# Kernel optimization log

Measured on AMD Instinct MI355X. Metric: run time of the kernel, lower is better.

The kernel has to match this reference:

```python
import jax, jax.numpy as jnp
import numpy as np

BS, K, VOCAB = 128, 8, 50257

def setup_inputs() -> dict:
    key = jax.random.key(0)
    k1, k2, k3, k4 = jax.random.split(key, 4)
    logits = jax.random.normal(k1, (BS * K + BS, VOCAB), dtype=jnp.float32)
    temperatures = jax.random.uniform(k2, (BS,), minval=0.5, maxval=1.5, dtype=jnp.float32)
    draft_token_ids = jax.random.randint(k3, (BS, K), 0, VOCAB)
    dlogits = jax.random.normal(k4, (BS * K, VOCAB), dtype=jnp.float32)
    draft_probs = jax.nn.softmax(dlogits, axis=-1)  # valid draft distribution per row
    return {"draft_token_ids": draft_token_ids, "logits": logits,
            "temperatures": temperatures, "draft_probs": draft_probs}

def reference(draft_token_ids, logits, temperatures, draft_probs):
    bs, k = draft_token_ids.shape
    vocab = logits.shape[-1]
    n_draft = bs * k
    nkey = jax.random.key(42)
    ku, kg_rec, kg_bonus = jax.random.split(nkey, 3)

    # --- bonus token sampling (inner `sampler`): categorical over softmax(logits/temp)
    # via the Gumbel-max trick (equivalent to torch.multinomial on the softmax probs)
    bonus_logits = logits[n_draft:] / temperatures[:, None]            # [bs, vocab]
    g_bonus = jax.random.gumbel(kg_bonus, (bs, vocab), dtype=jnp.float32)
    bonus_ids = jnp.argmax(bonus_logits + g_bonus, axis=-1)           # [bs]

    # --- target probabilities for draft positions
    target_logits = logits[:n_draft].reshape(bs, k, vocab) / temperatures[:, None, None]
    target_probs = jax.nn.softmax(target_logits, axis=-1)              # [bs,k,vocab]
    dprobs = draft_probs.reshape(bs, k, vocab)

    # per-position probs of the proposed draft token
    p_t = jnp.take_along_axis(target_probs, draft_token_ids[..., None], axis=-1)[..., 0]
    p_d = jnp.take_along_axis(dprobs, draft_token_ids[..., None], axis=-1)[..., 0]
    accept_prob = jnp.where(p_d > 0.0,
                            jnp.minimum(1.0, p_t / jnp.maximum(p_d, 1e-30)),
                            0.0)                                       # [bs,k]
    u = jax.random.uniform(ku, (bs, k), dtype=jnp.float32)
    accept = u <= accept_prob                                          # [bs,k]

    # accepted prefix length: number of leading accepts
    prefix = jnp.cumprod(accept.astype(jnp.int32), axis=1)
    n_acc = prefix.sum(axis=1)                                         # [bs] in [0,k]

    # --- recovery sampling: multinomial over clamp(target - draft, 0), renormalized;
    # fall back to target_probs if residual mass is zero. Gumbel-max on log weights
    # is invariant to normalization, so no explicit division by the mass is needed.
    rec = jnp.maximum(target_probs - dprobs, 0.0)                      # [bs,k,vocab]
    mass = rec.sum(axis=-1, keepdims=True)
    rec_dist = jnp.where(mass > 0.0, rec, target_probs)
    g_rec = jax.random.gumbel(kg_rec, (bs, k, vocab), dtype=jnp.float32)
    recovered = jnp.argmax(jnp.log(jnp.maximum(rec_dist, 1e-30)) + g_rec, axis=-1)  # [bs,k]

    # recovered token at the first rejected position (clipped gather; masked below)
    rej_pos = jnp.minimum(n_acc, k - 1)
    rec_at = jnp.take_along_axis(recovered, rej_pos[:, None], axis=1)[:, 0]  # [bs]

    # --- assemble padded output [bs, k+1]: accepted draft prefix, then either
    # recovered token (if a rejection occurred) or bonus token (all accepted); -1 pad.
    pos = jnp.arange(k + 1)[None, :]
    draft_pad = jnp.concatenate(
        [draft_token_ids, jnp.zeros((bs, 1), dtype=draft_token_ids.dtype)], axis=1)
    final_tok = jnp.where(n_acc[:, None] == k, bonus_ids[:, None], rec_at[:, None])
    out = jnp.where(pos < n_acc[:, None], draft_pad,
                    jnp.where(pos == n_acc[:, None], final_tok, -1))
    return out
```

## Files before the change

kernel.cpp:

```cpp
#include <hip/hip_runtime.h>
#include <cstdint>

#define VOCAB  50257
#define BSZ    128
#define KD     8
#define NDRAFT (BSZ * KD)
#define SEG    16
#define SEGLEN 3142

typedef float fx4 __attribute__((ext_vector_type(4)));

__device__ inline fx4 ntload4(const fx4* p) {
  return __builtin_nontemporal_load(p);
}

__host__ __device__ inline uint32_t rotl32(uint32_t x, int r) {
  return (x << r) | (x >> (32 - r));
}

__host__ __device__ inline void threefry2x32(uint32_t k0, uint32_t k1,
                                             uint32_t x0, uint32_t x1,
                                             uint32_t& o0, uint32_t& o1) {
  uint32_t ks2 = k0 ^ k1 ^ 0x1BD11BDAu;
  x0 += k0; x1 += k1;
  x0 += x1; x1 = rotl32(x1, 13); x1 ^= x0;
  x0 += x1; x1 = rotl32(x1, 15); x1 ^= x0;
  x0 += x1; x1 = rotl32(x1, 26); x1 ^= x0;
  x0 += x1; x1 = rotl32(x1,  6); x1 ^= x0;
  x0 += k1; x1 += ks2 + 1u;
  x0 += x1; x1 = rotl32(x1, 17); x1 ^= x0;
  x0 += x1; x1 = rotl32(x1, 29); x1 ^= x0;
  x0 += x1; x1 = rotl32(x1, 16); x1 ^= x0;
  x0 += x1; x1 = rotl32(x1, 24); x1 ^= x0;
  x0 += ks2; x1 += k0 + 2u;
  x0 += x1; x1 = rotl32(x1, 13); x1 ^= x0;
  x0 += x1; x1 = rotl32(x1, 15); x1 ^= x0;
  x0 += x1; x1 = rotl32(x1, 26); x1 ^= x0;
  x0 += x1; x1 = rotl32(x1,  6); x1 ^= x0;
  x0 += k0; x1 += k1 + 3u;
  x0 += x1; x1 = rotl32(x1, 17); x1 ^= x0;
  x0 += x1; x1 = rotl32(x1, 29); x1 ^= x0;
  x0 += x1; x1 = rotl32(x1, 16); x1 ^= x0;
  x0 += x1; x1 = rotl32(x1, 24); x1 ^= x0;
  x0 += k1; x1 += ks2 + 4u;
  x0 += x1; x1 = rotl32(x1, 13); x1 ^= x0;
  x0 += x1; x1 = rotl32(x1, 15); x1 ^= x0;
  x0 += x1; x1 = rotl32(x1, 26); x1 ^= x0;
  x0 += x1; x1 = rotl32(x1,  6); x1 ^= x0;
  x0 += ks2; x1 += k0 + 5u;
  o0 = x0; o1 = x1;
}

__device__ inline uint32_t tf_bits32(uint32_t k0, uint32_t k1, uint64_t idx) {
  uint32_t o0, o1;
  threefry2x32(k0, k1, (uint32_t)(idx >> 32), (uint32_t)idx, o0, o1);
  return o0 ^ o1;
}

__device__ inline float bits_to_f01(uint32_t bits) {
  return __uint_as_float((bits >> 9) | 0x3f800000u) - 1.0f;
}

__device__ inline float gumbel_fast(uint32_t bits) {
  const float tiny = 1.1754943508222875e-38f;
  float u = fmaxf(tiny, bits_to_f01(bits) + tiny);
  return -__logf(-__logf(u));
}

__device__ inline unsigned long long pack_si(float s, int idx) {
  uint32_t u = __float_as_uint(s);
  u = (u & 0x80000000u) ? ~u : (u | 0x80000000u);
  return ((unsigned long long)u << 32) | (uint32_t)(VOCAB - idx);
}
__device__ inline int unpack_idx(unsigned long long p) {
  return VOCAB - (int)(p & 0xFFFFFFFFu);
}

__device__ inline int nacc_from_bits(int bits) {
  return __builtin_ctz(~bits & 0x1FF);
}

__global__ __launch_bounds__(256) void k_stats_bonus(
    const float* __restrict__ logits, const float* __restrict__ temps,
    const int* __restrict__ dtok, const float* __restrict__ dprobs,
    float* __restrict__ row_max, float* __restrict__ row_sum,
    int* __restrict__ acc_bits,
    unsigned long long* __restrict__ bon_pack,
    uint32_t kb0, uint32_t kb1, uint32_t ku0, uint32_t ku1) {
  int tid = threadIdx.x;
  if ((int)blockIdx.x < NDRAFT) {
    int row = blockIdx.x;
    int b = row >> 3;
    float t = temps[b];
    float inv_t = 1.0f / t;
    const float* x = logits + (size_t)row * VOCAB;

    int tok = 0; float x_tok = 0.0f, pd_tok = 0.0f;
    if (tid == 0) {
      tok    = dtok[row];
      x_tok  = x[tok];
      pd_tok = dprobs[(size_t)row * VOCAB + tok];
    }

    float m_t = -INFINITY, s_t = 0.0f;
    auto upd = [&](float val) {
      float xs = val * inv_t;
      float nm = fmaxf(m_t, xs);
      s_t = s_t * __expf(m_t - nm) + __expf(xs - nm);
      m_t = nm;
    };
    int pre = (4 - (row & 3)) & 3;
    if (tid < pre) upd(x[tid]);
    int nv = (VOCAB - pre) >> 2;
    const fx4* xv = (const fx4*)(x + pre);
    int i = tid;
    for (; i + 256 < nv; i += 512) {
      fx4 q0 = ntload4(xv + i);
      fx4 q1 = ntload4(xv + i + 256);
      upd(q0.x); upd(q0.y); upd(q0.z); upd(q0.w);
      upd(q1.x); upd(q1.y); upd(q1.z); upd(q1.w);
    }
    for (; i < nv; i += 256) {
      fx4 q = ntload4(xv + i);
      upd(q.x); upd(q.y); upd(q.z); upd(q.w);
    }
    for (int v = pre + 4 * nv + tid; v < VOCAB; v += 256) upd(x[v]);

    __shared__ float sm[256], ss[256];
    sm[tid] = m_t; ss[tid] = s_t;
    __syncthreads();
    for (int st = 128; st > 0; st >>= 1) {
      if (tid < st) {
        float m2 = sm[tid + st], s2 = ss[tid + st];
        float M = fmaxf(sm[tid], m2);
        ss[tid] = ss[tid] * __expf(sm[tid] - M) + s2 * __expf(m2 - M);
        sm[tid] = M;
      }
      __syncthreads();
    }
    if (tid == 0) {
      float M = sm[0], S = ss[0];
      row_max[row] = M; row_sum[row] = S;
      float xt = x_tok / t;
      float pt = expf(xt - M) / S;
      float ap = (pd_tok > 0.0f) ? fminf(1.0f, pt / fmaxf(pd_tok, 1e-30f)) : 0.0f;
      float u  = bits_to_f01(tf_bits32(ku0, ku1, (uint64_t)row));
      if (u <= ap) atomicOr(&acc_bits[b], 1 << (row & 7));
    }
  } else {
    int r = blockIdx.x - NDRAFT;
    int b = r >> 4, seg = r & 15;
    int v0 = seg * SEGLEN;
    int v1 = v0 + SEGLEN; if (v1 > VOCAB) v1 = VOCAB;
    float inv_t = 1.0f / temps[b];
    const float* x = logits + (size_t)(NDRAFT + b) * VOCAB;
    uint64_t base = (uint64_t)b * VOCAB;
    float bv = -INFINITY; int bi = VOCAB;
    for (int v = v0 + tid; v < v1; v += 256) {
      float sc = x[v] * inv_t + gumbel_fast(tf_bits32(kb0, kb1, base + v));
      if (sc > bv) { bv = sc; bi = v; }
    }
    __shared__ unsigned long long sp[256];
    sp[tid] = pack_si(bv, bi);
    __syncthreads();
    for (int st = 128; st > 0; st >>= 1) {
      if (tid < st) { if (sp[tid + st] > sp[tid]) sp[tid] = sp[tid + st]; }
      __syncthreads();
    }
    if (tid == 0) atomicMax(&bon_pack[b], sp[0]);
  }
}

__global__ __launch_bounds__(256) void k_recover(
    const float* __restrict__ logits, const float* __restrict__ temps,
    const float* __restrict__ dprobs,
    const float* __restrict__ row_max, const float* __restrict__ row_sum,
    const int* __restrict__ acc_bits,
    unsigned long long* __restrict__ rec_pc,
    unsigned long long* __restrict__ rec_pp,
    int* __restrict__ rec_any,
    uint32_t kr0, uint32_t kr1) {
  int r = blockIdx.x;
  int b = r >> 4, seg = r & 15;
  int n = nacc_from_bits(acc_bits[b]);
  if (n >= KD) return;
  int tid = threadIdx.x;
  int row = b * KD + n;
  float inv_t = 1.0f / temps[b];
  float m = row_max[row];
  float inv_s = 1.0f / row_sum[row];
  const float* x  = logits + (size_t)row * VOCAB;
  const float* pd = dprobs + (size_t)row * VOCAB;
  uint64_t base = (uint64_t)row * VOCAB;

  float bc = -INFINITY, bp = -INFINITY;
  int ic = VOCAB, ip = VOCAB, any = 0;

  auto proc = [&](float xval, float pdval, int v) {
    float pt = __expf(xval * inv_t - m) * inv_s;
    float diff = pt - pdval;
    if (diff > 0.0f) any = 1;
    float g = gumbel_fast(tf_bits32(kr0, kr1, base + (uint64_t)v));
    float scc = __logf(fmaxf(fmaxf(diff, 0.0f), 1e-30f)) + g;
    float scp = __logf(fmaxf(pt, 1e-30f)) + g;
    if (scc > bc) { bc = scc; ic = v; }
    if (scp > bp) { bp = scp; ip = v; }
  };

  int pre = (4 - (row & 3)) & 3;
  int nv = (VOCAB - pre) >> 2;
  const fx4* xv = (const fx4*)(x + pre);
  const fx4* pv = (const fx4*)(pd + pre);
  int per = (nv + SEG - 1) / SEG;
  int s0 = seg * per;
  int s1 = s0 + per; if (s1 > nv) s1 = nv;
  for (int i = s0 + tid; i < s1; i += 256) {
    fx4 qx = ntload4(xv + i);
    fx4 qp = ntload4(pv + i);
    int v = pre + 4 * i;
    proc(qx.x, qp.x, v);
    proc(qx.y, qp.y, v + 1);
    proc(qx.z, qp.z, v + 2);
    proc(qx.w, qp.w, v + 3);
  }
  if (seg == 0) {
    if (tid < pre) proc(x[tid], pd[tid], tid);
  }
  if (seg == SEG - 1) {
    for (int v = pre + 4 * nv + tid; v < VOCAB; v += 256) proc(x[v], pd[v], v);
  }

  __shared__ unsigned long long sp[256];
  __shared__ int sa[256];
  sp[tid] = pack_si(bc, ic); sa[tid] = any;
  __syncthreads();
  for (int st = 128; st > 0; st >>= 1) {
    if (tid < st) {
      if (sp[tid + st] > sp[tid]) sp[tid] = sp[tid + st];
      sa[tid] |= sa[tid + st];
    }
    __syncthreads();
  }
  if (tid == 0) {
    atomicMax(&rec_pc[b], sp[0]);
    if (sa[0]) atomicOr(&rec_any[b], 1);
  }
  __syncthreads();
  sp[tid] = pack_si(bp, ip);
  __syncthreads();
  for (int st = 128; st > 0; st >>= 1) {
    if (tid < st) { if (sp[tid + st] > sp[tid]) sp[tid] = sp[tid + st]; }
    __syncthreads();
  }
  if (tid == 0) atomicMax(&rec_pp[b], sp[0]);
}

__global__ void k_final(const int* __restrict__ dtok,
                        const int* __restrict__ acc_bits,
                        const unsigned long long* __restrict__ bon_pack,
                        const unsigned long long* __restrict__ rec_pc,
                        const unsigned long long* __restrict__ rec_pp,
                        const int* __restrict__ rec_any,
                        int* __restrict__ out) {
  int idx = blockIdx.x * blockDim.x + threadIdx.x;
  if (idx >= BSZ * (KD + 1)) return;
  int b = idx / (KD + 1), p = idx % (KD + 1);
  int n = nacc_from_bits(acc_bits[b]);
  int val;
  if (p < n)       val = dtok[b * KD + p];
  else if (p == n) {
    if (n == KD) val = unpack_idx(bon_pack[b]);
    else         val = unpack_idx(rec_any[b] ? rec_pc[b] : rec_pp[b]);
  }
  else             val = -1;
  out[idx] = val;
}

extern "C" void kernel_launch(void* const* d_in, const int* in_sizes, int n_in,
                              void* d_out, int out_size, void* d_ws, size_t ws_size,
                              hipStream_t stream) {
  const int*   dtok   = (const int*)  d_in[0];
  const float* logits = (const float*)d_in[1];
  const float* temps  = (const float*)d_in[2];
  const float* dprobs = (const float*)d_in[3];
  int* out = (int*)d_out;

  unsigned long long* bon_pack = (unsigned long long*)d_ws;
  unsigned long long* rec_pc   = bon_pack + BSZ;
  unsigned long long* rec_pp   = rec_pc + BSZ;
  int*   rec_any  = (int*)(rec_pp + BSZ);
  int*   acc_bits = rec_any + BSZ;
  float* row_max  = (float*)(acc_bits + BSZ);
  float* row_sum  = row_max + NDRAFT;

  uint32_t ku0, ku1, kr0, kr1, kb0, kb1;
  threefry2x32(0u, 42u, 0u, 0u, ku0, ku1);
  threefry2x32(0u, 42u, 0u, 1u, kr0, kr1);
  threefry2x32(0u, 42u, 0u, 2u, kb0, kb1);

  hipMemsetAsync(d_ws, 0, (size_t)(3 * BSZ * 8 + 2 * BSZ * 4), stream);

  k_stats_bonus<<<NDRAFT + BSZ * SEG, 256, 0, stream>>>(
      logits, temps, dtok, dprobs, row_max, row_sum, acc_bits, bon_pack,
      kb0, kb1, ku0, ku1);
  k_recover<<<BSZ * SEG, 256, 0, stream>>>(logits, temps, dprobs,
                                           row_max, row_sum, acc_bits,
                                           rec_pc, rec_pp, rec_any, kr0, kr1);
  k_final<<<(BSZ * (KD + 1) + 255) / 256, 256, 0, stream>>>(
      dtok, acc_bits, bon_pack, rec_pc, rec_pp, rec_any, out);
}
```

Before: 425.7 us.

## Skip bonus sampling for rejected batches and replace atomics with per-segment partials

Moves bonus-token sampling out of the stats kernel and into the recover kernel, so its blocks run only when all draft tokens of a batch are accepted. Acceptance is written as per-row flags instead of atomic bitmasks, and the block results are written to per-segment partial arrays that the final kernel reduces, which removes the memset and the global atomics. The stats loop is unrolled to four vector loads per iteration. In exchange, the bonus work now waits for the stats kernel instead of overlapping with it, and the final kernel does the reduction serially with one thread per batch.

```diff
diff --git a/kernel.cpp b/kernel.cpp
--- a/kernel.cpp
+++ b/kernel.cpp
@@ -76,80 +76,102 @@
   return VOCAB - (int)(p & 0xFFFFFFFFu);
 }
 
-__device__ inline int nacc_from_bits(int bits) {
-  return __builtin_ctz(~bits & 0x1FF);
-}
-
-__global__ __launch_bounds__(256) void k_stats_bonus(
+__device__ inline int nacc_flags(const int* __restrict__ f, int b) {
+  int n = 0;
+#pragma unroll
+  for (int j = 0; j < KD; j++) {
+    if (f[b * KD + j]) n++;
+    else break;
+  }
+  return n;
+}
+
+__global__ __launch_bounds__(256) void k_stats(
     const float* __restrict__ logits, const float* __restrict__ temps,
     const int* __restrict__ dtok, const float* __restrict__ dprobs,
     float* __restrict__ row_max, float* __restrict__ row_sum,
-    int* __restrict__ acc_bits,
-    unsigned long long* __restrict__ bon_pack,
-    uint32_t kb0, uint32_t kb1, uint32_t ku0, uint32_t ku1) {
+    int* __restrict__ acc_flag,
+    uint32_t ku0, uint32_t ku1) {
   int tid = threadIdx.x;
-  if ((int)blockIdx.x < NDRAFT) {
-    int row = blockIdx.x;
-    int b = row >> 3;
-    float t = temps[b];
-    float inv_t = 1.0f / t;
-    const float* x = logits + (size_t)row * VOCAB;
-
-    int tok = 0; float x_tok = 0.0f, pd_tok = 0.0f;
-    if (tid == 0) {
-      tok    = dtok[row];
-      x_tok  = x[tok];
-      pd_tok = dprobs[(size_t)row * VOCAB + tok];
-    }
-
-    float m_t = -INFINITY, s_t = 0.0f;
-    auto upd = [&](float val) {
-      float xs = val * inv_t;
-      float nm = fmaxf(m_t, xs);
-      s_t = s_t * __expf(m_t - nm) + __expf(xs - nm);
-      m_t = nm;
-    };
-    int pre = (4 - (row & 3)) & 3;
-    if (tid < pre) upd(x[tid]);
-    int nv = (VOCAB - pre) >> 2;
-    const fx4* xv = (const fx4*)(x + pre);
-    int i = tid;
-    for (; i + 256 < nv; i += 512) {
-      fx4 q0 = ntload4(xv + i);
-      fx4 q1 = ntload4(xv + i + 256);
-      upd(q0.x); upd(q0.y); upd(q0.z); upd(q0.w);
-      upd(q1.x); upd(q1.y); upd(q1.z); upd(q1.w);
-    }
-    for (; i < nv; i += 256) {
-      fx4 q = ntload4(xv + i);
-      upd(q.x); upd(q.y); upd(q.z); upd(q.w);
-    }
-    for (int v = pre + 4 * nv + tid; v < VOCAB; v += 256) upd(x[v]);
-
-    __shared__ float sm[256], ss[256];
-    sm[tid] = m_t; ss[tid] = s_t;
-    __syncthreads();
-    for (int st = 128; st > 0; st >>= 1) {
-      if (tid < st) {
-        float m2 = sm[tid + st], s2 = ss[tid + st];
-        float M = fmaxf(sm[tid], m2);
-        ss[tid] = ss[tid] * __expf(sm[tid] - M) + s2 * __expf(m2 - M);
-        sm[tid] = M;
-      }
-      __syncthreads();
-    }
-    if (tid == 0) {
-      float M = sm[0], S = ss[0];
-      row_max[row] = M; row_sum[row] = S;
-      float xt = x_tok / t;
-      float pt = expf(xt - M) / S;
-      float ap = (pd_tok > 0.0f) ? fminf(1.0f, pt / fmaxf(pd_tok, 1e-30f)) : 0.0f;
-      float u  = bits_to_f01(tf_bits32(ku0, ku1, (uint64_t)row));
-      if (u <= ap) atomicOr(&acc_bits[b], 1 << (row & 7));
-    }
-  } else {
-    int r = blockIdx.x - NDRAFT;
+  int row = blockIdx.x;
+  int b = row >> 3;
+  float t = temps[b];
+  float inv_t = 1.0f / t;
+  const float* x = logits + (size_t)row * VOCAB;
+
+  int tok = 0; float x_tok = 0.0f, pd_tok = 0.0f;
+  if (tid == 0) {
+    tok    = dtok[row];
+    x_tok  = x[tok];
+    pd_tok = dprobs[(size_t)row * VOCAB + tok];
+  }
+
+  float m_t = -INFINITY, s_t = 0.0f;
+  auto upd = [&](float val) {
+    float xs = val * inv_t;
+    float nm = fmaxf(m_t, xs);
+    s_t = s_t * __expf(m_t - nm) + __expf(xs - nm);
+    m_t = nm;
+  };
+  int pre = (4 - (row & 3)) & 3;
+  if (tid < pre) upd(x[tid]);
+  int nv = (VOCAB - pre) >> 2;
+  const fx4* xv = (const fx4*)(x + pre);
+  int i = tid;
+  for (; i + 768 < nv; i += 1024) {
+    fx4 q0 = ntload4(xv + i);
+    fx4 q1 = ntload4(xv + i + 256);
+    fx4 q2 = ntload4(xv + i + 512);
+    fx4 q3 = ntload4(xv + i + 768);
+    upd(q0.x); upd(q0.y); upd(q0.z); upd(q0.w);
+    upd(q1.x); upd(q1.y); upd(q1.z); upd(q1.w);
+    upd(q2.x); upd(q2.y); upd(q2.z); upd(q2.w);
+    upd(q3.x); upd(q3.y); upd(q3.z); upd(q3.w);
+  }
+  for (; i < nv; i += 256) {
+    fx4 q = ntload4(xv + i);
+    upd(q.x); upd(q.y); upd(q.z); upd(q.w);
+  }
+  for (int v = pre + 4 * nv + tid; v < VOCAB; v += 256) upd(x[v]);
+
+  __shared__ float sm[256], ss[256];
+  sm[tid] = m_t; ss[tid] = s_t;
+  __syncthreads();
+  for (int st = 128; st > 0; st >>= 1) {
+    if (tid < st) {
+      float m2 = sm[tid + st], s2 = ss[tid + st];
+      float M = fmaxf(sm[tid], m2);
+      ss[tid] = ss[tid] * __expf(sm[tid] - M) + s2 * __expf(m2 - M);
+      sm[tid] = M;
+    }
+    __syncthreads();
+  }
+  if (tid == 0) {
+    float M = sm[0], S = ss[0];
+    row_max[row] = M; row_sum[row] = S;
+    float xt = x_tok / t;
+    float pt = expf(xt - M) / S;
+    float ap = (pd_tok > 0.0f) ? fminf(1.0f, pt / fmaxf(pd_tok, 1e-30f)) : 0.0f;
+    float u  = bits_to_f01(tf_bits32(ku0, ku1, (uint64_t)row));
+    acc_flag[row] = (u <= ap) ? 1 : 0;
+  }
+}
+
+__global__ __launch_bounds__(256) void k_bonus_recover(
+    const float* __restrict__ logits, const float* __restrict__ temps,
+    const float* __restrict__ dprobs,
+    const float* __restrict__ row_max, const float* __restrict__ row_sum,
+    const int* __restrict__ acc_flag,
+    unsigned long long* __restrict__ bon_part,
+    unsigned long long* __restrict__ rec_pc_part,
+    unsigned long long* __restrict__ rec_pp_part,
+    int* __restrict__ rec_any_part,
+    uint32_t kb0, uint32_t kb1, uint32_t kr0, uint32_t kr1) {
+  int tid = threadIdx.x;
+  if ((int)blockIdx.x < BSZ * SEG) {
+    int r = blockIdx.x;
     int b = r >> 4, seg = r & 15;
+    if (nacc_flags(acc_flag, b) != KD) return;
     int v0 = seg * SEGLEN;
     int v1 = v0 + SEGLEN; if (v1 > VOCAB) v1 = VOCAB;
     float inv_t = 1.0f / temps[b];
@@ -167,113 +189,120 @@
       if (tid < st) { if (sp[tid + st] > sp[tid]) sp[tid] = sp[tid + st]; }
       __syncthreads();
     }
-    if (tid == 0) atomicMax(&bon_pack[b], sp[0]);
-  }
-}
-
-__global__ __launch_bounds__(256) void k_recover(
-    const float* __restrict__ logits, const float* __restrict__ temps,
-    const float* __restrict__ dprobs,
-    const float* __restrict__ row_max, const float* __restrict__ row_sum,
-    const int* __restrict__ acc_bits,
-    unsigned long long* __restrict__ rec_pc,
-    unsigned long long* __restrict__ rec_pp,
-    int* __restrict__ rec_any,
-    uint32_t kr0, uint32_t kr1) {
-  int r = blockIdx.x;
-  int b = r >> 4, seg = r & 15;
-  int n = nacc_from_bits(acc_bits[b]);
-  if (n >= KD) return;
-  int tid = threadIdx.x;
-  int row = b * KD + n;
-  float inv_t = 1.0f / temps[b];
-  float m = row_max[row];
-  float inv_s = 1.0f / row_sum[row];
-  const float* x  = logits + (size_t)row * VOCAB;
-  const float* pd = dprobs + (size_t)row * VOCAB;
-  uint64_t base = (uint64_t)row * VOCAB;
-
-  float bc = -INFINITY, bp = -INFINITY;
-  int ic = VOCAB, ip = VOCAB, any = 0;
-
-  auto proc = [&](float xval, float pdval, int v) {
-    float pt = __expf(xval * inv_t - m) * inv_s;
-    float diff = pt - pdval;
-    if (diff > 0.0f) any = 1;
-    float g = gumbel_fast(tf_bits32(kr0, kr1, base + (uint64_t)v));
-    float scc = __logf(fmaxf(fmaxf(diff, 0.0f), 1e-30f)) + g;
-    float scp = __logf(fmaxf(pt, 1e-30f)) + g;
-    if (scc > bc) { bc = scc; ic = v; }
-    if (scp > bp) { bp = scp; ip = v; }
-  };
-
-  int pre = (4 - (row & 3)) & 3;
-  int nv = (VOCAB - pre) >> 2;
-  const fx4* xv = (const fx4*)(x + pre);
-  const fx4* pv = (const fx4*)(pd + pre);
-  int per = (nv + SEG - 1) / SEG;
-  int s0 = seg * per;
-  int s1 = s0 + per; if (s1 > nv) s1 = nv;
-  for (int i = s0 + tid; i < s1; i += 256) {
-    fx4 qx = ntload4(xv + i);
-    fx4 qp = ntload4(pv + i);
-    int v = pre + 4 * i;
-    proc(qx.x, qp.x, v);
-    proc(qx.y, qp.y, v + 1);
-    proc(qx.z, qp.z, v + 2);
-    proc(qx.w, qp.w, v + 3);
-  }
-  if (seg == 0) {
-    if (tid < pre) proc(x[tid], pd[tid], tid);
-  }
-  if (seg == SEG - 1) {
-    for (int v = pre + 4 * nv + tid; v < VOCAB; v += 256) proc(x[v], pd[v], v);
-  }
-
-  __shared__ unsigned long long sp[256];
-  __shared__ int sa[256];
-  sp[tid] = pack_si(bc, ic); sa[tid] = any;
-  __syncthreads();
-  for (int st = 128; st > 0; st >>= 1) {
-    if (tid < st) {
-      if (sp[tid + st] > sp[tid]) sp[tid] = sp[tid + st];
-      sa[tid] |= sa[tid + st];
-    }
-    __syncthreads();
-  }
-  if (tid == 0) {
-    atomicMax(&rec_pc[b], sp[0]);
-    if (sa[0]) atomicOr(&rec_any[b], 1);
-  }
-  __syncthreads();
-  sp[tid] = pack_si(bp, ip);
-  __syncthreads();
-  for (int st = 128; st > 0; st >>= 1) {
-    if (tid < st) { if (sp[tid + st] > sp[tid]) sp[tid] = sp[tid + st]; }
-    __syncthreads();
-  }
-  if (tid == 0) atomicMax(&rec_pp[b], sp[0]);
+    if (tid == 0) bon_part[r] = sp[0];
+  } else {
+    int r = blockIdx.x - BSZ * SEG;
+    int b = r >> 4, seg = r & 15;
+    int n = nacc_flags(acc_flag, b);
+    if (n >= KD) return;
+    int row = b * KD + n;
+    float inv_t = 1.0f / temps[b];
+    float m = row_max[row];
+    float inv_s = 1.0f / row_sum[row];
+    const float* x  = logits + (size_t)row * VOCAB;
+    const float* pd = dprobs + (size_t)row * VOCAB;
+    uint64_t base = (uint64_t)row * VOCAB;
+
+    float bc = -INFINITY, bp = -INFINITY;
+    int ic = VOCAB, ip = VOCAB, any = 0;
+
+    auto proc = [&](float xval, float pdval, int v) {
+      float pt = __expf(xval * inv_t - m) * inv_s;
+      float diff = pt - pdval;
+      if (diff > 0.0f) any = 1;
+      float g = gumbel_fast(tf_bits32(kr0, kr1, base + (uint64_t)v));
+      float scc = __logf(fmaxf(fmaxf(diff, 0.0f), 1e-30f)) + g;
+      float scp = __logf(fmaxf(pt, 1e-30f)) + g;
+      if (scc > bc) { bc = scc; ic = v; }
+      if (scp > bp) { bp = scp; ip = v; }
+    };
+
+    int pre = (4 - (row & 3)) & 3;
+    int nv = (VOCAB - pre) >> 2;
+    const fx4* xv = (const fx4*)(x + pre);
+    const fx4* pv = (const fx4*)(pd + pre);
+    int per = (nv + SEG - 1) / SEG;
+    int s0 = seg * per;
+    int s1 = s0 + per; if (s1 > nv) s1 = nv;
+    for (int i = s0 + tid; i < s1; i += 256) {
+      fx4 qx = ntload4(xv + i);
+      fx4 qp = ntload4(pv + i);
+      int v = pre + 4 * i;
+      proc(qx.x, qp.x, v);
+      proc(qx.y, qp.y, v + 1);
+      proc(qx.z, qp.z, v + 2);
+      proc(qx.w, qp.w, v + 3);
+    }
+    if (seg == 0) {
+      if (tid < pre) proc(x[tid], pd[tid], tid);
+    }
+    if (seg == SEG - 1) {
+      for (int v = pre + 4 * nv + tid; v < VOCAB; v += 256) proc(x[v], pd[v], v);
+    }
+
+    __shared__ unsigned long long sp[256];
+    __shared__ int sa[256];
+    sp[tid] = pack_si(bc, ic); sa[tid] = any;
+    __syncthreads();
+    for (int st = 128; st > 0; st >>= 1) {
+      if (tid < st) {
+        if (sp[tid + st] > sp[tid]) sp[tid] = sp[tid + st];
+        sa[tid] |= sa[tid + st];
+      }
+      __syncthreads();
+    }
+    if (tid == 0) { rec_pc_part[r] = sp[0]; rec_any_part[r] = sa[0]; }
+    __syncthreads();
+    sp[tid] = pack_si(bp, ip);
+    __syncthreads();
+    for (int st = 128; st > 0; st >>= 1) {
+      if (tid < st) { if (sp[tid + st] > sp[tid]) sp[tid] = sp[tid + st]; }
+      __syncthreads();
+    }
+    if (tid == 0) rec_pp_part[r] = sp[0];
+  }
 }
 
 __global__ void k_final(const int* __restrict__ dtok,
-                        const int* __restrict__ acc_bits,
-                        const unsigned long long* __restrict__ bon_pack,
-                        const unsigned long long* __restrict__ rec_pc,
-                        const unsigned long long* __restrict__ rec_pp,
-                        const int* __restrict__ rec_any,
+                        const int* __restrict__ acc_flag,
+                        const unsigned long long* __restrict__ bon_part,
+                        const unsigned long long* __restrict__ rec_pc_part,
+                        const unsigned long long* __restrict__ rec_pp_part,
+                        const int* __restrict__ rec_any_part,
                         int* __restrict__ out) {
-  int idx = blockIdx.x * blockDim.x + threadIdx.x;
-  if (idx >= BSZ * (KD + 1)) return;
-  int b = idx / (KD + 1), p = idx % (KD + 1);
-  int n = nacc_from_bits(acc_bits[b]);
-  int val;
-  if (p < n)       val = dtok[b * KD + p];
-  else if (p == n) {
-    if (n == KD) val = unpack_idx(bon_pack[b]);
-    else         val = unpack_idx(rec_any[b] ? rec_pc[b] : rec_pp[b]);
-  }
-  else             val = -1;
-  out[idx] = val;
+  int b = blockIdx.x * blockDim.x + threadIdx.x;
+  if (b >= BSZ) return;
+  int n = nacc_flags(acc_flag, b);
+  int tok_final;
+  if (n == KD) {
+    unsigned long long m = 0;
+#pragma unroll
+    for (int s = 0; s < SEG; s++) {
+      unsigned long long v = bon_part[b * SEG + s];
+      if (v > m) m = v;
+    }
+    tok_final = unpack_idx(m);
+  } else {
+    unsigned long long mc = 0, mp = 0; int any = 0;
+#pragma unroll
+    for (int s = 0; s < SEG; s++) {
+      int idx = b * SEG + s;
+      unsigned long long vc = rec_pc_part[idx];
+      unsigned long long vp = rec_pp_part[idx];
+      if (vc > mc) mc = vc;
+      if (vp > mp) mp = vp;
+      any |= rec_any_part[idx];
+    }
+    tok_final = unpack_idx(any ? mc : mp);
+  }
+#pragma unroll
+  for (int p = 0; p <= KD; p++) {
+    int val;
+    if (p < n)       val = dtok[b * KD + p];
+    else if (p == n) val = tok_final;
+    else             val = -1;
+    out[b * (KD + 1) + p] = val;
+  }
 }
 
 extern "C" void kernel_launch(void* const* d_in, const int* in_sizes, int n_in,
@@ -285,27 +314,25 @@
   const float* dprobs = (const float*)d_in[3];
   int* out = (int*)d_out;
 
-  unsigned long long* bon_pack = (unsigned long long*)d_ws;
-  unsigned long long* rec_pc   = bon_pack + BSZ;
-  unsigned long long* rec_pp   = rec_pc + BSZ;
-  int*   rec_any  = (int*)(rec_pp + BSZ);
-  int*   acc_bits = rec_any + BSZ;
-  float* row_max  = (float*)(acc_bits + BSZ);
+  float* row_max  = (float*)d_ws;
   float* row_sum  = row_max + NDRAFT;
+  int*   acc_flag = (int*)(row_sum + NDRAFT);
+  unsigned long long* bon_part    = (unsigned long long*)(acc_flag + NDRAFT);
+  unsigned long long* rec_pc_part = bon_part + BSZ * SEG;
+  unsigned long long* rec_pp_part = rec_pc_part + BSZ * SEG;
+  int*   rec_any_part = (int*)(rec_pp_part + BSZ * SEG);
 
   uint32_t ku0, ku1, kr0, kr1, kb0, kb1;
   threefry2x32(0u, 42u, 0u, 0u, ku0, ku1);
   threefry2x32(0u, 42u, 0u, 1u, kr0, kr1);
   threefry2x32(0u, 42u, 0u, 2u, kb0, kb1);
 
-  hipMemsetAsync(d_ws, 0, (size_t)(3 * BSZ * 8 + 2 * BSZ * 4), stream);
-
-  k_stats_bonus<<<NDRAFT + BSZ * SEG, 256, 0, stream>>>(
-      logits, temps, dtok, dprobs, row_max, row_sum, acc_bits, bon_pack,
-      kb0, kb1, ku0, ku1);
-  k_recover<<<BSZ * SEG, 256, 0, stream>>>(logits, temps, dprobs,
-                                           row_max, row_sum, acc_bits,
-                                           rec_pc, rec_pp, rec_any, kr0, kr1);
-  k_final<<<(BSZ * (KD + 1) + 255) / 256, 256, 0, stream>>>(
-      dtok, acc_bits, bon_pack, rec_pc, rec_pp, rec_any, out);
-}
+  k_stats<<<NDRAFT, 256, 0, stream>>>(
+      logits, temps, dtok, dprobs, row_max, row_sum, acc_flag, ku0, ku1);
+  k_bonus_recover<<<2 * BSZ * SEG, 256, 0, stream>>>(
+      logits, temps, dprobs, row_max, row_sum, acc_flag,
+      bon_part, rec_pc_part, rec_pp_part, rec_any_part,
+      kb0, kb1, kr0, kr1);
+  k_final<<<1, BSZ, 0, stream>>>(
+      dtok, acc_flag, bon_part, rec_pc_part, rec_pp_part, rec_any_part, out);
+}
```

Measured after the change: 412.6 us. -3.1%, faster.
